# Optimization experiments

Measured on AMD Instinct MI355X. Metric: run time of the kernel, lower is better.

The kernel has to match this reference:

```python
import jax, jax.numpy as jnp
import numpy as np

N, M, E, DIM, H = 50000, 50000, 640000, 128, 8
DH = DIM // H
EPS = 1e-5

def _prelu(x, alpha):
    return jnp.where(x >= 0, x, alpha * x)

def setup_inputs() -> dict:
    key0 = jax.random.key(0)
    ks = jax.random.split(key0, 12)
    s = 1.0 / np.sqrt(DIM)
    return {
        "query": jax.random.normal(ks[0], (N, DIM), jnp.float32),
        "key": jax.random.normal(ks[1], (M, DIM), jnp.float32),
        "value": jax.random.normal(ks[2], (M, DIM), jnp.float32),
        "query_idx": jax.random.randint(ks[3], (E,), 0, N),
        "key_idx": jax.random.randint(ks[4], (E,), 0, M),
        "Wq": jax.random.normal(ks[5], (DIM, DIM), jnp.float32) * s,
        "bq": jnp.zeros((DIM,), jnp.float32),
        "Wk": jax.random.normal(ks[6], (DIM, DIM), jnp.float32) * s,
        "bk": jnp.zeros((DIM,), jnp.float32),
        "Wv": jax.random.normal(ks[7], (DIM, DIM), jnp.float32) * s,
        "bv": jnp.zeros((DIM,), jnp.float32),
        "Wp": jax.random.normal(ks[8], (DIM, DIM), jnp.float32) * s,
        "bp": jnp.zeros((DIM,), jnp.float32),
        "a": jax.random.normal(ks[9], (1, H, DH), jnp.float32) * 0.1,
        "alpha": jnp.full((1,), 0.25, jnp.float32),
        "gamma": jnp.ones((DIM,), jnp.float32),
        "beta": jnp.zeros((DIM,), jnp.float32),
    }

def reference(query, key, value, query_idx, key_idx, Wq, bq, Wk, bk, Wv, bv, Wp, bp, a, alpha, gamma, beta):
    n = query.shape[0]
    # projections (node-level, then gather per edge; linear commutes with gather)
    Qq = query @ Wq + bq            # [N, DIM]
    Kq = query @ Wk + bk            # [N, DIM] (self-attn key)
    Kk = key @ Wk + bk              # [M, DIM]
    Vq = query @ Wv + bv            # [N, DIM]
    Vv = value @ Wv + bv            # [M, DIM]
    # self-attention score per query node: [N, H, 1]
    attn_qq = (a * _prelu(Qq + Kq, alpha).reshape(n, H, DH)).sum(-1, keepdims=True)
    # per-edge additive attention score: [E, H, 1]
    e_feat = _prelu(Qq[query_idx] + Kk[key_idx], alpha)
    attn_e = (a * e_feat.reshape(-1, H, DH)).sum(-1, keepdims=True)
    # stable softmax over irregular query groups (include self)
    max_attn = jax.lax.stop_gradient(attn_qq.at[query_idx].max(attn_e))
    exp_qq = jnp.exp(attn_qq - max_attn)                 # [N, H, 1]
    exp_e = jnp.exp(attn_e - max_attn[query_idx])        # [E, H, 1]
    denom = exp_qq.at[query_idx].add(exp_e)              # [N, H, 1]
    denom = jnp.where(denom == 0, 1.0, denom)
    # weighted value scatter-sum (value_idx == key_idx)
    msg = exp_qq * Vq.reshape(n, H, DH)
    msg = msg.at[query_idx].add(exp_e * Vv[key_idx].reshape(-1, H, DH))
    out = (msg / denom).reshape(n, DIM) @ Wp + bp
    res = query + out
    mu = res.mean(-1, keepdims=True)
    var = res.var(-1, keepdims=True)
    return gamma * (res - mu) / jnp.sqrt(var + EPS) + beta
```

## Files before the change

### kernel.cpp

```cpp
#include <hip/hip_runtime.h>
#include <math.h>

#define DIM 128
#define NH 8
#define LN_EPS 1e-5f
#define NEGINF -3.0e38f

using bf16x8 = __attribute__((ext_vector_type(8))) short;
using f32x4  = __attribute__((ext_vector_type(4))) float;

__device__ __forceinline__ short f2bf(float f) {
    unsigned u = __float_as_uint(f);
    unsigned r = (u + 0x7fffu + ((u >> 16) & 1u)) >> 16;
    return (short)r;
}
__device__ __forceinline__ float bflo(unsigned u) { return __uint_as_float(u << 16); }
__device__ __forceinline__ float bfhi(unsigned u) { return __uint_as_float(u & 0xffff0000u); }

__device__ __forceinline__ unsigned cvt_pk_bf16(float lo, float hi) {
    unsigned r;
    asm("v_cvt_pk_bf16_f32 %0, %1, %2" : "=v"(r) : "v"(lo), "v"(hi));
    return r;
}

__device__ __forceinline__ float swz_xor1(float x) {
    return __int_as_float(__builtin_amdgcn_ds_swizzle(__float_as_int(x), 0x041F));
}
__device__ __forceinline__ float swz_xor16(float x) {
    return __int_as_float(__builtin_amdgcn_ds_swizzle(__float_as_int(x), 0x401F));
}
__device__ __forceinline__ float swz_xor32(float x) {
    return __shfl_xor(x, 32);
}

__global__ __launch_bounds__(256) void setup_kernel(
    const float* __restrict__ W0, const float* __restrict__ W1,
    const float* __restrict__ W2, const float* __restrict__ W3,
    short* __restrict__ P0, short* __restrict__ P1,
    short* __restrict__ P2, short* __restrict__ P3,
    const int* __restrict__ qidx, int* __restrict__ counts, int E)
{
    if (blockIdx.x < 32) {
        const int id = blockIdx.x * 256 + threadIdx.x;
        const int mat = id >> 11;
        const int rem = id & 2047;
        const int ks = rem >> 9;
        const int ct = (rem >> 6) & 7;
        const int lane = rem & 63;
        const int lr = lane & 15, lg = lane >> 4;
        const float* W = mat == 0 ? W0 : mat == 1 ? W1 : mat == 2 ? W2 : W3;
        short* P = mat == 0 ? P0 : mat == 1 ? P1 : mat == 2 ? P2 : P3;
        short v[8];
        #pragma unroll
        for (int r = 0; r < 8; ++r)
            v[r] = f2bf(W[(ks * 32 + lg * 8 + r) * DIM + ct * 16 + lr]);
        *(bf16x8*)&P[(size_t)((ks * 8 + ct) * 64 + lane) * 8] = *(bf16x8*)v;
    } else {
        const int b = blockIdx.x - 32;
        for (int e = b * 256 + threadIdx.x; e < E; e += 1024 * 256)
            atomicAdd(&counts[qidx[e]], 1);
    }
}

__global__ __launch_bounds__(256) void proj_all_mfma(
    const float* __restrict__ query,
    const float* __restrict__ key, const float* __restrict__ value,
    const short* __restrict__ Wqp, const short* __restrict__ Wkp, const short* __restrict__ Wvp,
    const float* __restrict__ bq, const float* __restrict__ bk, const float* __restrict__ bv,
    short* __restrict__ QKV16, short* __restrict__ KV16, int N, int M, int nb)
{
    __shared__ short tile[4][16][260];
    const int wid = threadIdx.x >> 6, lane = threadIdx.x & 63;
    const int lr = lane & 15, lg = lane >> 4;

    if ((int)blockIdx.x < nb) {
        const int row0 = ((int)blockIdx.x * 4 + wid) * 16;
        if (row0 >= N) return;
        const int arow = row0 + lr;
        const bool rowok = arow < N;

        bf16x8 afrag[4];
        #pragma unroll
        for (int ks = 0; ks < 4; ++ks) {
            float t[8] = {0.f,0.f,0.f,0.f,0.f,0.f,0.f,0.f};
            if (rowok) {
                *(float4*)&t[0] = *(const float4*)&query[(size_t)arow * DIM + ks * 32 + lg * 8];
                *(float4*)&t[4] = *(const float4*)&query[(size_t)arow * DIM + ks * 32 + lg * 8 + 4];
            }
            union { bf16x8 v; unsigned u[4]; } a;
            a.u[0] = cvt_pk_bf16(t[0], t[1]);
            a.u[1] = cvt_pk_bf16(t[2], t[3]);
            a.u[2] = cvt_pk_bf16(t[4], t[5]);
            a.u[3] = cvt_pk_bf16(t[6], t[7]);
            afrag[ks] = a.v;
        }
        unsigned* qkvout = (unsigned*)QKV16;

        #pragma unroll 2
        for (int ct = 0; ct < 8; ++ct) {
            f32x4 aq = (f32x4)0.f, ak = (f32x4)0.f;
            #pragma unroll
            for (int ks = 0; ks < 4; ++ks) {
                const size_t bo = (size_t)((ks * 8 + ct) * 64 + lane) * 8;
                aq = __builtin_amdgcn_mfma_f32_16x16x32_bf16(afrag[ks], *(const bf16x8*)&Wqp[bo], aq, 0, 0, 0);
                ak = __builtin_amdgcn_mfma_f32_16x16x32_bf16(afrag[ks], *(const bf16x8*)&Wkp[bo], ak, 0, 0, 0);
            }
            const int col = ct * 16 + lr;
            const float bqv = bq[col], bkv = bk[col];
            #pragma unroll
            for (int r = 0; r < 4; ++r) {
                const int row = lg * 4 + r;
                tile[wid][row][col]       = (short)cvt_pk_bf16(aq[r] + bqv, 0.f);
                tile[wid][row][128 + col] = (short)cvt_pk_bf16(ak[r] + bkv, 0.f);
            }
        }
        #pragma unroll
        for (int rr = 0; rr < 16; ++rr) {
            const int grow = row0 + rr;
            if (grow < N) {
                #pragma unroll
                for (int s = 0; s < 2; ++s) {
                    const short2 pr = *(const short2*)&tile[wid][rr][s * 128 + lane * 2];
                    qkvout[(size_t)grow * 192 + s * 64 + lane] =
                        (unsigned)(unsigned short)pr.x | ((unsigned)(unsigned short)pr.y << 16);
                }
            }
        }

        #pragma unroll 2
        for (int ct = 0; ct < 8; ++ct) {
            f32x4 acv = (f32x4)0.f;
            #pragma unroll
            for (int ks = 0; ks < 4; ++ks) {
                const size_t bo = (size_t)((ks * 8 + ct) * 64 + lane) * 8;
                acv = __builtin_amdgcn_mfma_f32_16x16x32_bf16(afrag[ks], *(const bf16x8*)&Wvp[bo], acv, 0, 0, 0);
            }
            const int col = ct * 16 + lr;
            const float bvv = bv[col];
            #pragma unroll
            for (int r = 0; r < 4; ++r)
                tile[wid][lg * 4 + r][col] = (short)cvt_pk_bf16(acv[r] + bvv, 0.f);
        }
        #pragma unroll
        for (int rr = 0; rr < 16; ++rr) {
            const int grow = row0 + rr;
            if (grow < N) {
                const short2 pr = *(const short2*)&tile[wid][rr][lane * 2];
                qkvout[(size_t)grow * 192 + 128 + lane] =
                    (unsigned)(unsigned short)pr.x | ((unsigned)(unsigned short)pr.y << 16);
            }
        }
    } else {
        const int row0 = (((int)blockIdx.x - nb) * 4 + wid) * 16;
        if (row0 >= M) return;
        const int arow = row0 + lr;
        const bool rowok = arow < M;
        unsigned* kvout = (unsigned*)KV16;

        bf16x8 afK[4], afV[4];
        #pragma unroll
        for (int ks = 0; ks < 4; ++ks) {
            float tk[8] = {0.f,0.f,0.f,0.f,0.f,0.f,0.f,0.f};
            float tv[8] = {0.f,0.f,0.f,0.f,0.f,0.f,0.f,0.f};
            if (rowok) {
                *(float4*)&tk[0] = *(const float4*)&key[(size_t)arow * DIM + ks * 32 + lg * 8];
                *(float4*)&tk[4] = *(const float4*)&key[(size_t)arow * DIM + ks * 32 + lg * 8 + 4];
                *(float4*)&tv[0] = *(const float4*)&value[(size_t)arow * DIM + ks * 32 + lg * 8];
                *(float4*)&tv[4] = *(const float4*)&value[(size_t)arow * DIM + ks * 32 + lg * 8 + 4];
            }
            union { bf16x8 v; unsigned u[4]; } a, b;
            a.u[0] = cvt_pk_bf16(tk[0], tk[1]);
            a.u[1] = cvt_pk_bf16(tk[2], tk[3]);
            a.u[2] = cvt_pk_bf16(tk[4], tk[5]);
            a.u[3] = cvt_pk_bf16(tk[6], tk[7]);
            b.u[0] = cvt_pk_bf16(tv[0], tv[1]);
            b.u[1] = cvt_pk_bf16(tv[2], tv[3]);
            b.u[2] = cvt_pk_bf16(tv[4], tv[5]);
            b.u[3] = cvt_pk_bf16(tv[6], tv[7]);
            afK[ks] = a.v; afV[ks] = b.v;
        }

        #pragma unroll 2
        for (int ct = 0; ct < 8; ++ct) {
            f32x4 ack = (f32x4)0.f, acv = (f32x4)0.f;
            #pragma unroll
            for (int ks = 0; ks < 4; ++ks) {
                const size_t bo = (size_t)((ks * 8 + ct) * 64 + lane) * 8;
                ack = __builtin_amdgcn_mfma_f32_16x16x32_bf16(afK[ks], *(const bf16x8*)&Wkp[bo], ack, 0, 0, 0);
                acv = __builtin_amdgcn_mfma_f32_16x16x32_bf16(afV[ks], *(const bf16x8*)&Wvp[bo], acv, 0, 0, 0);
            }
            const int col = ct * 16 + lr;
            const float bkv = bk[col], bvv = bv[col];
            #pragma unroll
            for (int r = 0; r < 4; ++r) {
                const int row = lg * 4 + r;
                tile[wid][row][col]       = (short)cvt_pk_bf16(ack[r] + bkv, 0.f);
                tile[wid][row][128 + col] = (short)cvt_pk_bf16(acv[r] + bvv, 0.f);
            }
        }
        #pragma unroll
        for (int rr = 0; rr < 16; ++rr) {
            const int grow = row0 + rr;
            if (grow < M) {
                #pragma unroll
                for (int s = 0; s < 2; ++s) {
                    const short2 pr = *(const short2*)&tile[wid][rr][s * 128 + lane * 2];
                    kvout[(size_t)grow * 128 + s * 64 + lane] =
                        (unsigned)(unsigned short)pr.x | ((unsigned)(unsigned short)pr.y << 16);
                }
            }
        }
    }
}

__global__ __launch_bounds__(256) void scan1_kernel(const int* __restrict__ counts,
                                                    int* __restrict__ bsum, int N)
{
    __shared__ int sh[256];
    int i = blockIdx.x * 256 + threadIdx.x;
    sh[threadIdx.x] = (i < N) ? counts[i] : 0;
    __syncthreads();
    #pragma unroll
    for (int off = 128; off; off >>= 1) {
        if (threadIdx.x < off) sh[threadIdx.x] += sh[threadIdx.x + off];
        __syncthreads();
    }
    if (threadIdx.x == 0) bsum[blockIdx.x] = sh[0];
}

__global__ __launch_bounds__(256) void scan2_kernel(const int* __restrict__ bsum,
                                                    int* __restrict__ boff, int B)
{
    int t = threadIdx.x;
    if (B > 256) {
        if (t == 0) { int run = 0; for (int i = 0; i < B; ++i) { int v = bsum[i]; boff[i] = run; run += v; } }
        return;
    }
    __shared__ int sh[256];
    int v = (t < B) ? bsum[t] : 0;
    sh[t] = v;
    __syncthreads();
    for (int off = 1; off < 256; off <<= 1) {
        int x = (t >= off) ? sh[t - off] : 0;
        __syncthreads();
        sh[t] += x;
        __syncthreads();
    }
    if (t < B) boff[t] = sh[t] - v;
}

__global__ __launch_bounds__(256) void scan3_kernel(const int* __restrict__ counts,
                                                    const int* __restrict__ boff,
                                                    int* __restrict__ offsets,
                                                    int* __restrict__ cursor,
                                                    int N, int E)
{
    __shared__ int sh[256];
    int t = threadIdx.x;
    int i = blockIdx.x * 256 + t;
    int v = (i < N) ? counts[i] : 0;
    sh[t] = v;
    __syncthreads();
    for (int off = 1; off < 256; off <<= 1) {
        int x = (t >= off) ? sh[t - off] : 0;
        __syncthreads();
        sh[t] += x;
        __syncthreads();
    }
    int base = boff[blockIdx.x];
    if (i < N) {
        int o = base + sh[t] - v;
        offsets[i] = o;
        cursor[i] = o;
    }
    if (i == 0) offsets[N] = E;
}

__global__ void fill_kernel(const int* __restrict__ qidx, const int* __restrict__ kidx,
                            int* __restrict__ cursor, int* __restrict__ ksorted, int E)
{
    for (int e = blockIdx.x * blockDim.x + threadIdx.x; e < E; e += gridDim.x * blockDim.x) {
        int q = qidx[e];
        int pos = atomicAdd(&cursor[q], 1);
        ksorted[pos] = kidx[e];
    }
}

__global__ __launch_bounds__(256) void edge_agg_kernel(
    const short* __restrict__ QKV16,
    const short* __restrict__ KV16,
    const int* __restrict__ ksorted, const int* __restrict__ offsets,
    const float* __restrict__ avec, const float* __restrict__ alpha_p,
    short* __restrict__ msgn16, int N)
{
    const int lane = threadIdx.x & 63;
    const int wid  = threadIdx.x >> 6;
    const int e    = lane >> 4;
    const int sub  = lane & 15;

    const float al = alpha_p[0];
    const float r  = (1.f - al) / (1.f + al);
    const float s1 = (1.f + al) * 0.5f;

    float c[8];
    {
        const float4 a0 = *(const float4*)&avec[sub * 8];
        const float4 a1 = *(const float4*)&avec[sub * 8 + 4];
        c[0] = a0.x * s1; c[1] = a0.y * s1; c[2] = a0.z * s1; c[3] = a0.w * s1;
        c[4] = a1.x * s1; c[5] = a1.y * s1; c[6] = a1.z * s1; c[7] = a1.w * s1;
    }

    const char* KVb = (const char*)KV16;
    const unsigned subB = (unsigned)(sub * 16);
    const int wavesTotal = gridDim.x * 4;

    for (int n = blockIdx.x * 4 + wid; n < N; n += wavesTotal) {
        float q[8];
        {
            unsigned qd[4];
            *(uint4*)qd = *(const uint4*)&QKV16[(size_t)n * 384 + sub * 8];
            #pragma unroll
            for (int j = 0; j < 4; ++j) { q[2*j] = bflo(qd[j]); q[2*j+1] = bfhi(qd[j]); }
        }

        float m;
        {
            unsigned kq[4];
            *(uint4*)kq = *(const uint4*)&QKV16[(size_t)n * 384 + 128 + sub * 8];
            float sp = 0.f;
            #pragma unroll
            for (int j = 0; j < 4; ++j) {
                const float x0 = q[2*j]   + bflo(kq[j]);
                const float x1 = q[2*j+1] + bfhi(kq[j]);
                sp = fmaf(c[2*j],   fmaf(r, __builtin_fabsf(x0), x0), sp);
                sp = fmaf(c[2*j+1], fmaf(r, __builtin_fabsf(x1), x1), sp);
            }
            m = sp + swz_xor1(sp);
        }

        float acc[8];
        float den;
        if (e == 0) {
            unsigned vdi[4];
            *(uint4*)vdi = *(const uint4*)&QKV16[(size_t)n * 384 + 256 + sub * 8];
            #pragma unroll
            for (int j = 0; j < 4; ++j) { acc[2*j] = bflo(vdi[j]); acc[2*j+1] = bfhi(vdi[j]); }
            den = 1.f;
        } else {
            #pragma unroll
            for (int d = 0; d < 8; ++d) acc[d] = 0.f;
            den = 0.f;
        }

        const int p0 = offsets[n];
        const int p1 = offsets[n + 1];
        const int T  = (p1 - p0 + 3) >> 2;
        bool div = false;

        #define ROWLOAD(kd_, vd_, ki_)                                        \
            {                                                                 \
                const unsigned ob = (unsigned)(ki_) * 512u + subB;            \
                *(uint4*)(kd_) = *(const uint4*)(KVb + ob);                   \
                *(uint4*)(vd_) = *(const uint4*)(KVb + ob + 256);             \
            }

        unsigned kdA[4], vdA[4], kdB[4], vdB[4];
        unsigned kdC[4], vdC[4], kdD[4], vdD[4];
        bool vA, vB, vC, vD;
        int kiA, kiB, kiC, kiD;

        {
            int i0 = p0 + e,      i1 = p0 + 4 + e;
            int i2 = p0 + 8 + e,  i3 = p0 + 12 + e;
            vA = i0 < p1; vB = i1 < p1; vC = i2 < p1; vD = i3 < p1;
            const int k0 = vA ? ksorted[i0] : 0;
            const int k1 = vB ? ksorted[i1] : 0;
            const int k2 = vC ? ksorted[i2] : 0;
            const int k3 = vD ? ksorted[i3] : 0;
            ROWLOAD(kdA, vdA, k0); ROWLOAD(kdB, vdB, k1);
            ROWLOAD(kdC, vdC, k2); ROWLOAD(kdD, vdD, k3);
            int j0 = p0 + 16 + e, j1 = p0 + 20 + e;
            int j2 = p0 + 24 + e, j3 = p0 + 28 + e;
            kiA = (j0 < p1) ? ksorted[j0] : 0;
            kiB = (j1 < p1) ? ksorted[j1] : 0;
            kiC = (j2 < p1) ? ksorted[j2] : 0;
            kiD = (j3 < p1) ? ksorted[j3] : 0;
        }

        #define COMPUTE(kd_, vd_, vflag)                                      \
            {                                                                 \
                float sp = 0.f;                                               \
                _Pragma("unroll")                                             \
                for (int j = 0; j < 4; ++j) {                                 \
                    const float x0 = q[2*j]   + bflo(kd_[j]);                 \
                    const float x1 = q[2*j+1] + bfhi(kd_[j]);                 \
                    const float t0 = fmaf(r, __builtin_fabsf(x0), x0);        \
                    const float t1 = fmaf(r, __builtin_fabsf(x1), x1);        \
                    sp = fmaf(c[2*j], t0, sp);                                \
                    sp = fmaf(c[2*j+1], t1, sp);                              \
                }                                                             \
                const float sf = sp + swz_xor1(sp);                           \
                const float s = (vflag) ? sf : NEGINF;                        \
                const float d_ = s - m;                                       \
                if (__any(d_ > 8.f)) {                                        \
                    div = true;                                               \
                    const float nm = fmaxf(m, s);                             \
                    const float cc = __expf(m - nm);                          \
                    const float w = __expf(s - nm);                           \
                    den = den * cc + w;                                       \
                    _Pragma("unroll")                                         \
                    for (int j = 0; j < 4; ++j) {                             \
                        acc[2*j]   = fmaf(acc[2*j],   cc, w * bflo(vd_[j])); \
                        acc[2*j+1] = fmaf(acc[2*j+1], cc, w * bfhi(vd_[j])); \
                    }                                                         \
                    m = nm;                                                   \
                } else {                                                      \
                    const float w = __expf(d_);                               \
                    den += w;                                                 \
                    _Pragma("unroll")                                         \
                    for (int j = 0; j < 4; ++j) {                             \
                        acc[2*j]   = fmaf(w, bflo(vd_[j]), acc[2*j]);         \
                        acc[2*j+1] = fmaf(w, bfhi(vd_[j]), acc[2*j+1]);       \
                    }                                                         \
                }                                                             \
            }

        #define RELOAD(kd_, vd_, vflag, ki_, st4, st8)                        \
            {                                                                 \
                vflag = (p0 + (st4) * 4 + e) < p1;                            \
                ROWLOAD(kd_, vd_, ki_);                                       \
                const int fi = p0 + (st8) * 4 + e;                            \
                ki_ = (fi < p1) ? ksorted[fi] : 0;                            \
            }

        #pragma unroll 1
        for (int t = 0; t < T; t += 4) {
            COMPUTE(kdA, vdA, vA); RELOAD(kdA, vdA, vA, kiA, t + 4, t + 8);
            COMPUTE(kdB, vdB, vB); RELOAD(kdB, vdB, vB, kiB, t + 5, t + 9);
            COMPUTE(kdC, vdC, vC); RELOAD(kdC, vdC, vC, kiC, t + 6, t + 10);
            COMPUTE(kdD, vdD, vD); RELOAD(kdD, vdD, vD, kiD, t + 7, t + 11);
        }
        #undef COMPUTE
        #undef RELOAD
        #undef ROWLOAD

        #define MERGE_ROUND(SWZ)                                    \
            {                                                       \
                const float m2 = SWZ(m);                            \
                const float den2 = SWZ(den);                        \
                const float nm = fmaxf(m, m2);                      \
                const float ca = __expf(m - nm);                    \
                const float cb = __expf(m2 - nm);                   \
                den = den * ca + den2 * cb;                         \
                _Pragma("unroll")                                   \
                for (int d = 0; d < 8; ++d)                         \
                    acc[d] = acc[d] * ca + SWZ(acc[d]) * cb;        \
                m = nm;                                             \
            }
        #define SUM_ROUND(SWZ)                                      \
            {                                                       \
                den += SWZ(den);                                    \
                _Pragma("unroll")                                   \
                for (int d = 0; d < 8; ++d) acc[d] += SWZ(acc[d]);  \
            }
        if (div) {
            MERGE_ROUND(swz_xor16);
            MERGE_ROUND(swz_xor32);
        } else {
            SUM_ROUND(swz_xor16);
            SUM_ROUND(swz_xor32);
        }
        #undef MERGE_ROUND
        #undef SUM_ROUND

        if (e == 0) {
            const float inv = 1.f / den;
            unsigned u[4];
            #pragma unroll
            for (int j = 0; j < 4; ++j)
                u[j] = cvt_pk_bf16(acc[2*j] * inv, acc[2*j+1] * inv);
            *(uint4*)&msgn16[(size_t)n * DIM + sub * 8] = *(uint4*)u;
        }
    }
}

__global__ __launch_bounds__(256) void out_ln_mfma(
    const short* __restrict__ msgn16, const short* __restrict__ Wpp,
    const float* __restrict__ bp, const float* __restrict__ query,
    const float* __restrict__ gamma, const float* __restrict__ beta,
    float* __restrict__ out, int N)
{
    __shared__ float ys[64][130];
    const int wid = threadIdx.x >> 6, lane = threadIdx.x & 63;
    const int rowbase = blockIdx.x * 64;
    const int row0 = rowbase + wid * 16;
    const int lr = lane & 15, lg = lane >> 4;

    if (row0 < N) {
        bf16x8 afrag[4];
        const int arow = row0 + lr;
        const bool rowok = arow < N;
        #pragma unroll
        for (int ks = 0; ks < 4; ++ks) {
            if (rowok)
                afrag[ks] = *(const bf16x8*)&msgn16[(size_t)arow * DIM + ks * 32 + lg * 8];
            else {
                bf16x8 z;
                #pragma unroll
                for (int j = 0; j < 8; ++j) z[j] = 0;
                afrag[ks] = z;
            }
        }
        #pragma unroll 2
        for (int ct = 0; ct < 8; ++ct) {
            f32x4 acc = (f32x4)0.f;
            #pragma unroll
            for (int ks = 0; ks < 4; ++ks) {
                const size_t bo = (size_t)((ks * 8 + ct) * 64 + lane) * 8;
                acc = __builtin_amdgcn_mfma_f32_16x16x32_bf16(afrag[ks], *(const bf16x8*)&Wpp[bo], acc, 0, 0, 0);
            }
            const int col = ct * 16 + lr;
            const float bpv = bp[col];
            #pragma unroll
            for (int r = 0; r < 4; ++r)
                ys[wid * 16 + lg * 4 + r][col] = acc[r] + bpv;
        }
    }
    __syncthreads();

    for (int rr = 0; rr < 16; ++rr) {
        const int r = wid * 16 + rr;
        const int grow = rowbase + r;
        if (grow >= N) break;
        const float y1 = ys[r][lane], y2 = ys[r][lane + 64];
        const float q1 = query[(size_t)grow * DIM + lane];
        const float q2 = query[(size_t)grow * DIM + lane + 64];
        const float r1 = y1 + q1, r2 = y2 + q2;
        float s = r1 + r2;
        float ss = r1 * r1 + r2 * r2;
        #pragma unroll
        for (int off = 32; off; off >>= 1) {
            s += __shfl_xor(s, off);
            ss += __shfl_xor(ss, off);
        }
        const float mu = s * (1.f / DIM);
        const float var = ss * (1.f / DIM) - mu * mu;
        const float rstd = rsqrtf(var + LN_EPS);
        out[(size_t)grow * DIM + lane] = gamma[lane] * (r1 - mu) * rstd + beta[lane];
        out[(size_t)grow * DIM + lane + 64] = gamma[lane + 64] * (r2 - mu) * rstd + beta[lane + 64];
    }
}

extern "C" void kernel_launch(void* const* d_in, const int* in_sizes, int n_in,
                              void* d_out, int out_size, void* d_ws, size_t ws_size,
                              hipStream_t stream) {
    const float* query = (const float*)d_in[0];
    const float* key   = (const float*)d_in[1];
    const float* value = (const float*)d_in[2];
    const int* query_idx = (const int*)d_in[3];
    const int* key_idx   = (const int*)d_in[4];
    const float* Wq = (const float*)d_in[5];
    const float* bq = (const float*)d_in[6];
    const float* Wk = (const float*)d_in[7];
    const float* bk = (const float*)d_in[8];
    const float* Wv = (const float*)d_in[9];
    const float* bv = (const float*)d_in[10];
    const float* Wp = (const float*)d_in[11];
    const float* bp = (const float*)d_in[12];
    const float* avec  = (const float*)d_in[13];
    const float* alpha = (const float*)d_in[14];
    const float* gamma = (const float*)d_in[15];
    const float* beta  = (const float*)d_in[16];
    float* out = (float*)d_out;

    const int N = in_sizes[0] / DIM;
    const int M = in_sizes[1] / DIM;
    const int E = in_sizes[3];

    short* sp = (short*)d_ws;
    short* QKV16 = sp;  sp += (size_t)N * 384;
    short* KV16 = sp;   sp += (size_t)M * 256;
    short* msgn16 = sp; sp += (size_t)N * DIM;
    short* Wqp = sp;    sp += DIM * DIM;
    short* Wkp = sp;    sp += DIM * DIM;
    short* Wvp = sp;    sp += DIM * DIM;
    short* Wpp = sp;    sp += DIM * DIM;
    int* ip = (int*)(((size_t)sp + 15) & ~(size_t)15);
    int* counts  = ip;  ip += N;
    int* offsets = ip;  ip += N + 1;
    int* cursor  = ip;  ip += N;
    int* bsum    = ip;  ip += 4096;
    int* boff    = ip;  ip += 4096;
    int* ksorted = ip;  ip += E;

    const int B = (N + 255) / 256;
    const int nb = (N + 63) / 64;
    const int mb = (M + 63) / 64;

    hipMemsetAsync(counts, 0, (size_t)N * sizeof(int), stream);

    setup_kernel<<<1056, 256, 0, stream>>>(Wq, Wk, Wv, Wp, Wqp, Wkp, Wvp, Wpp,
                                           query_idx, counts, E);

    scan1_kernel<<<B, 256, 0, stream>>>(counts, bsum, N);
    scan2_kernel<<<1, 256, 0, stream>>>(bsum, boff, B);
    scan3_kernel<<<B, 256, 0, stream>>>(counts, boff, offsets, cursor, N, E);
    fill_kernel<<<1024, 256, 0, stream>>>(query_idx, key_idx, cursor, ksorted, E);

    proj_all_mfma<<<nb + mb, 256, 0, stream>>>(
        query, key, value, Wqp, Wkp, Wvp, bq, bk, bv,
        QKV16, KV16, N, M, nb);

    edge_agg_kernel<<<2048, 256, 0, stream>>>(
        QKV16, KV16, ksorted, offsets, avec, alpha, msgn16, N);

    out_ln_mfma<<<(N + 63) / 64, 256, 0, stream>>>(
        msgn16, Wpp, bp, query, gamma, beta, out, N);
}
```

Before: 209.5 us.

## Fuse self-attention score into projection kernel, drop stored Kq projection

The projection kernel now computes the per-node self-attention partial scores (a * prelu(Qq+Kq)) in its epilogue and writes them as 64 floats per node, instead of storing the bf16 Kq projection. Edge aggregation reads those partials and sums 8 of them per head rather than reloading Kq and recomputing the PReLU dot product. The query workspace shrinks from 384 to 256 shorts per row. The key/value branch is also split into two sequential passes so the shared tile can be halved. The trade-off is extra fp32 writes (256 B per node versus 256 B of bf16 Kq), so the intent is mainly less work and fewer registers in edge_agg, at roughly equal memory traffic.

```diff
diff --git a/kernel.cpp b/kernel.cpp
--- a/kernel.cpp
+++ b/kernel.cpp
@@ -8,6 +8,8 @@
 
 using bf16x8 = __attribute__((ext_vector_type(8))) short;
 using f32x4  = __attribute__((ext_vector_type(4))) float;
+
+__device__ __forceinline__ float prelu_f(float x, float al) { return x >= 0.f ? x : al * x; }
 
 __device__ __forceinline__ short f2bf(float f) {
     unsigned u = __float_as_uint(f);
@@ -67,9 +69,11 @@
     const float* __restrict__ key, const float* __restrict__ value,
     const short* __restrict__ Wqp, const short* __restrict__ Wkp, const short* __restrict__ Wvp,
     const float* __restrict__ bq, const float* __restrict__ bk, const float* __restrict__ bv,
-    short* __restrict__ QKV16, short* __restrict__ KV16, int N, int M, int nb)
-{
-    __shared__ short tile[4][16][260];
+    const float* __restrict__ avec, const float* __restrict__ alpha_p,
+    short* __restrict__ QV16, float* __restrict__ attnqq8,
+    short* __restrict__ KV16, int N, int M, int nb)
+{
+    __shared__ short tile[4][16][132];
     const int wid = threadIdx.x >> 6, lane = threadIdx.x & 63;
     const int lr = lane & 15, lg = lane >> 4;
 
@@ -94,7 +98,8 @@
             a.u[3] = cvt_pk_bf16(t[6], t[7]);
             afrag[ks] = a.v;
         }
-        unsigned* qkvout = (unsigned*)QKV16;
+        const float al = alpha_p[0];
+        unsigned* qvout = (unsigned*)QV16;
 
         #pragma unroll 2
         for (int ct = 0; ct < 8; ++ct) {
@@ -106,47 +111,50 @@
                 ak = __builtin_amdgcn_mfma_f32_16x16x32_bf16(afrag[ks], *(const bf16x8*)&Wkp[bo], ak, 0, 0, 0);
             }
             const int col = ct * 16 + lr;
-            const float bqv = bq[col], bkv = bk[col];
+            const float bqv = bq[col], bkv = bk[col], av = avec[col];
             #pragma unroll
             for (int r = 0; r < 4; ++r) {
                 const int row = lg * 4 + r;
-                tile[wid][row][col]       = (short)cvt_pk_bf16(aq[r] + bqv, 0.f);
-                tile[wid][row][128 + col] = (short)cvt_pk_bf16(ak[r] + bkv, 0.f);
-            }
-        }
-        #pragma unroll
-        for (int rr = 0; rr < 16; ++rr) {
-            const int grow = row0 + rr;
-            if (grow < N) {
-                #pragma unroll
-                for (int s = 0; s < 2; ++s) {
-                    const short2 pr = *(const short2*)&tile[wid][rr][s * 128 + lane * 2];
-                    qkvout[(size_t)grow * 192 + s * 64 + lane] =
-                        (unsigned)(unsigned short)pr.x | ((unsigned)(unsigned short)pr.y << 16);
-                }
-            }
-        }
-
-        #pragma unroll 2
-        for (int ct = 0; ct < 8; ++ct) {
-            f32x4 acv = (f32x4)0.f;
-            #pragma unroll
-            for (int ks = 0; ks < 4; ++ks) {
-                const size_t bo = (size_t)((ks * 8 + ct) * 64 + lane) * 8;
-                acv = __builtin_amdgcn_mfma_f32_16x16x32_bf16(afrag[ks], *(const bf16x8*)&Wvp[bo], acv, 0, 0, 0);
-            }
-            const int col = ct * 16 + lr;
-            const float bvv = bv[col];
-            #pragma unroll
-            for (int r = 0; r < 4; ++r)
-                tile[wid][lg * 4 + r][col] = (short)cvt_pk_bf16(acv[r] + bvv, 0.f);
+                const float qv = aq[r] + bqv;
+                const float kv = ak[r] + bkv;
+                float part = av * prelu_f(qv + kv, al);
+                part += swz_xor1(part);
+                const int grow = row0 + row;
+                if ((lr & 1) == 0 && grow < N)
+                    attnqq8[(size_t)grow * 64 + ct * 8 + (lr >> 1)] = part;
+                tile[wid][row][col] = (short)cvt_pk_bf16(qv, 0.f);
+            }
         }
         #pragma unroll
         for (int rr = 0; rr < 16; ++rr) {
             const int grow = row0 + rr;
             if (grow < N) {
                 const short2 pr = *(const short2*)&tile[wid][rr][lane * 2];
-                qkvout[(size_t)grow * 192 + 128 + lane] =
+                qvout[(size_t)grow * 128 + lane] =
+                    (unsigned)(unsigned short)pr.x | ((unsigned)(unsigned short)pr.y << 16);
+            }
+        }
+
+        #pragma unroll 2
+        for (int ct = 0; ct < 8; ++ct) {
+            f32x4 acv = (f32x4)0.f;
+            #pragma unroll
+            for (int ks = 0; ks < 4; ++ks) {
+                const size_t bo = (size_t)((ks * 8 + ct) * 64 + lane) * 8;
+                acv = __builtin_amdgcn_mfma_f32_16x16x32_bf16(afrag[ks], *(const bf16x8*)&Wvp[bo], acv, 0, 0, 0);
+            }
+            const int col = ct * 16 + lr;
+            const float bvv = bv[col];
+            #pragma unroll
+            for (int r = 0; r < 4; ++r)
+                tile[wid][lg * 4 + r][col] = (short)cvt_pk_bf16(acv[r] + bvv, 0.f);
+        }
+        #pragma unroll
+        for (int rr = 0; rr < 16; ++rr) {
+            const int grow = row0 + rr;
+            if (grow < N) {
+                const short2 pr = *(const short2*)&tile[wid][rr][lane * 2];
+                qvout[(size_t)grow * 128 + 64 + lane] =
                     (unsigned)(unsigned short)pr.x | ((unsigned)(unsigned short)pr.y << 16);
             }
         }
@@ -182,32 +190,49 @@
 
         #pragma unroll 2
         for (int ct = 0; ct < 8; ++ct) {
-            f32x4 ack = (f32x4)0.f, acv = (f32x4)0.f;
+            f32x4 ack = (f32x4)0.f;
             #pragma unroll
             for (int ks = 0; ks < 4; ++ks) {
                 const size_t bo = (size_t)((ks * 8 + ct) * 64 + lane) * 8;
                 ack = __builtin_amdgcn_mfma_f32_16x16x32_bf16(afK[ks], *(const bf16x8*)&Wkp[bo], ack, 0, 0, 0);
-                acv = __builtin_amdgcn_mfma_f32_16x16x32_bf16(afV[ks], *(const bf16x8*)&Wvp[bo], acv, 0, 0, 0);
             }
             const int col = ct * 16 + lr;
-            const float bkv = bk[col], bvv = bv[col];
-            #pragma unroll
-            for (int r = 0; r < 4; ++r) {
-                const int row = lg * 4 + r;
-                tile[wid][row][col]       = (short)cvt_pk_bf16(ack[r] + bkv, 0.f);
-                tile[wid][row][128 + col] = (short)cvt_pk_bf16(acv[r] + bvv, 0.f);
-            }
+            const float bkv = bk[col];
+            #pragma unroll
+            for (int r = 0; r < 4; ++r)
+                tile[wid][lg * 4 + r][col] = (short)cvt_pk_bf16(ack[r] + bkv, 0.f);
         }
         #pragma unroll
         for (int rr = 0; rr < 16; ++rr) {
             const int grow = row0 + rr;
             if (grow < M) {
-                #pragma unroll
-                for (int s = 0; s < 2; ++s) {
-                    const short2 pr = *(const short2*)&tile[wid][rr][s * 128 + lane * 2];
-                    kvout[(size_t)grow * 128 + s * 64 + lane] =
-                        (unsigned)(unsigned short)pr.x | ((unsigned)(unsigned short)pr.y << 16);
-                }
+                const short2 pr = *(const short2*)&tile[wid][rr][lane * 2];
+                kvout[(size_t)grow * 128 + lane] =
+                    (unsigned)(unsigned short)pr.x | ((unsigned)(unsigned short)pr.y << 16);
+            }
+        }
+
+        #pragma unroll 2
+        for (int ct = 0; ct < 8; ++ct) {
+            f32x4 acv = (f32x4)0.f;
+            #pragma unroll
+            for (int ks = 0; ks < 4; ++ks) {
+                const size_t bo = (size_t)((ks * 8 + ct) * 64 + lane) * 8;
+                acv = __builtin_amdgcn_mfma_f32_16x16x32_bf16(afV[ks], *(const bf16x8*)&Wvp[bo], acv, 0, 0, 0);
+            }
+            const int col = ct * 16 + lr;
+            const float bvv = bv[col];
+            #pragma unroll
+            for (int r = 0; r < 4; ++r)
+                tile[wid][lg * 4 + r][col] = (short)cvt_pk_bf16(acv[r] + bvv, 0.f);
+        }
+        #pragma unroll
+        for (int rr = 0; rr < 16; ++rr) {
+            const int grow = row0 + rr;
+            if (grow < M) {
+                const short2 pr = *(const short2*)&tile[wid][rr][lane * 2];
+                kvout[(size_t)grow * 128 + 64 + lane] =
+                    (unsigned)(unsigned short)pr.x | ((unsigned)(unsigned short)pr.y << 16);
             }
         }
     }
@@ -287,7 +312,7 @@
 }
 
 __global__ __launch_bounds__(256) void edge_agg_kernel(
-    const short* __restrict__ QKV16,
+    const short* __restrict__ QV16, const float* __restrict__ attnqq8,
     const short* __restrict__ KV16,
     const int* __restrict__ ksorted, const int* __restrict__ offsets,
     const float* __restrict__ avec, const float* __restrict__ alpha_p,
@@ -297,6 +322,7 @@
     const int wid  = threadIdx.x >> 6;
     const int e    = lane >> 4;
     const int sub  = lane & 15;
+    const int h    = sub >> 1;
 
     const float al = alpha_p[0];
     const float r  = (1.f - al) / (1.f + al);
@@ -318,31 +344,16 @@
         float q[8];
         {
             unsigned qd[4];
-            *(uint4*)qd = *(const uint4*)&QKV16[(size_t)n * 384 + sub * 8];
+            *(uint4*)qd = *(const uint4*)&QV16[(size_t)n * 256 + sub * 8];
             #pragma unroll
             for (int j = 0; j < 4; ++j) { q[2*j] = bflo(qd[j]); q[2*j+1] = bfhi(qd[j]); }
-        }
-
-        float m;
-        {
-            unsigned kq[4];
-            *(uint4*)kq = *(const uint4*)&QKV16[(size_t)n * 384 + 128 + sub * 8];
-            float sp = 0.f;
-            #pragma unroll
-            for (int j = 0; j < 4; ++j) {
-                const float x0 = q[2*j]   + bflo(kq[j]);
-                const float x1 = q[2*j+1] + bfhi(kq[j]);
-                sp = fmaf(c[2*j],   fmaf(r, __builtin_fabsf(x0), x0), sp);
-                sp = fmaf(c[2*j+1], fmaf(r, __builtin_fabsf(x1), x1), sp);
-            }
-            m = sp + swz_xor1(sp);
         }
 
         float acc[8];
         float den;
         if (e == 0) {
             unsigned vdi[4];
-            *(uint4*)vdi = *(const uint4*)&QKV16[(size_t)n * 384 + 256 + sub * 8];
+            *(uint4*)vdi = *(const uint4*)&QV16[(size_t)n * 256 + 128 + sub * 8];
             #pragma unroll
             for (int j = 0; j < 4; ++j) { acc[2*j] = bflo(vdi[j]); acc[2*j+1] = bfhi(vdi[j]); }
             den = 1.f;
@@ -350,6 +361,13 @@
             #pragma unroll
             for (int d = 0; d < 8; ++d) acc[d] = 0.f;
             den = 0.f;
+        }
+
+        float m;
+        {
+            const float4 a4 = *(const float4*)&attnqq8[(size_t)n * 64 + h * 8];
+            const float4 b4 = *(const float4*)&attnqq8[(size_t)n * 64 + h * 8 + 4];
+            m = ((a4.x + a4.y) + (a4.z + a4.w)) + ((b4.x + b4.y) + (b4.z + b4.w));
         }
 
         const int p0 = offsets[n];
@@ -577,8 +595,10 @@
     const int M = in_sizes[1] / DIM;
     const int E = in_sizes[3];
 
-    short* sp = (short*)d_ws;
-    short* QKV16 = sp;  sp += (size_t)N * 384;
+    float* f = (float*)d_ws;
+    float* attnqq8 = f; f += (size_t)N * 64;
+    short* sp = (short*)f;
+    short* QV16 = sp;   sp += (size_t)N * 256;
     short* KV16 = sp;   sp += (size_t)M * 256;
     short* msgn16 = sp; sp += (size_t)N * DIM;
     short* Wqp = sp;    sp += DIM * DIM;
@@ -608,11 +628,11 @@
     fill_kernel<<<1024, 256, 0, stream>>>(query_idx, key_idx, cursor, ksorted, E);
 
     proj_all_mfma<<<nb + mb, 256, 0, stream>>>(
-        query, key, value, Wqp, Wkp, Wvp, bq, bk, bv,
-        QKV16, KV16, N, M, nb);
+        query, key, value, Wqp, Wkp, Wvp, bq, bk, bv, avec, alpha,
+        QV16, attnqq8, KV16, N, M, nb);
 
     edge_agg_kernel<<<2048, 256, 0, stream>>>(
-        QKV16, KV16, ksorted, offsets, avec, alpha, msgn16, N);
+        QV16, attnqq8, KV16, ksorted, offsets, avec, alpha, msgn16, N);
 
     out_ln_mfma<<<(N + 63) / 64, 256, 0, stream>>>(
         msgn16, Wpp, bp, query, gamma, beta, out, N);
```

New measurement: 205.9 us. Within noise of the previous version (-1.7%).
